# Kernel tuning notes

Measured on AMD Instinct MI355X. Metric: run time of the kernel, lower is better.

The kernel has to match this reference:

```python
import jax, jax.numpy as jnp
import numpy as np

EPS_LN = 1e-5
EPS_NORM = 1e-12


def _bilinear_matrix(in_size, out_size):
    # align_corners=True bilinear interpolation as a dense (out,in) matrix
    pos = np.arange(out_size) * (in_size - 1) / (out_size - 1)
    lo = np.floor(pos).astype(np.int64)
    hi = np.minimum(lo + 1, in_size - 1)
    frac = (pos - lo).astype(np.float32)
    M = np.zeros((out_size, in_size), np.float32)
    M[np.arange(out_size), lo] += 1.0 - frac
    M[np.arange(out_size), hi] += frac
    return jnp.asarray(M)

_M20 = _bilinear_matrix(7, 20)  # [20,7]


def _upsample(x):
    # bilinear 7x7 -> 20x20, align_corners=True: separable matmuls
    return jnp.einsum('ih,jw,nchw->ncij', _M20, _M20, x)


def _conv2d(x, w, b, stride, pad):
    out = jax.lax.conv_general_dilated(
        x, w, window_strides=(stride, stride),
        padding=[(pad, pad), (pad, pad)],
        dimension_numbers=('NCHW', 'OIHW', 'NCHW'))
    return out + b[None, :, None, None]


def _crn(x, t, ln_w, ln_b, w_t, b_t, w_s, b_s, w_m, b_m, w_l, b_l, acc_w, acc_b):
    # LayerNorm over last two dims [7,7] with elementwise affine
    mu = x.mean(axis=(-2, -1), keepdims=True)
    var = x.var(axis=(-2, -1), keepdims=True)
    xn = (x - mu) * jax.lax.rsqrt(var + EPS_LN) * ln_w + ln_b
    up = _upsample(xn)                      # [N,512,20,20]
    xs = _conv2d(up, w_s, b_s, 3, 1)        # [N,32,7,7]
    xm = _conv2d(up, w_m, b_m, 5, 9)        # [N,32,7,7]
    xl = _conv2d(up, w_l, b_l, 2, 1)        # [N,20,7,7]
    tu = _upsample(t)
    tc = _conv2d(tu, w_t, b_t, 2, 0)        # [N,16,7,7]
    cat = jnp.concatenate([xs, xm, xl, tc], axis=1)  # [N,100,7,7]
    return _conv2d(cat, acc_w, acc_b, 1, 0)          # [N,1,7,7]


def setup_inputs() -> dict:
    key = jax.random.key(0)
    ks = jax.random.split(key, 16)
    N, C, K = 512, 512, 64
    centroids = jax.random.uniform(ks[0], (K, C), dtype=jnp.float32)
    return {
        'x': jax.random.normal(ks[1], (N, C, 7, 7), dtype=jnp.float32),
        't': jax.random.normal(ks[2], (N, C, 7, 7), dtype=jnp.float32),
        'centroids': centroids,
        'conv_w': 2.0 * 100.0 * centroids,
        'conv_b': -100.0 * jnp.linalg.norm(centroids, axis=1),
        'ln_w': jnp.ones((7, 7), jnp.float32),
        'ln_b': jnp.zeros((7, 7), jnp.float32),
        'w_t': jax.random.normal(ks[3], (16, 512, 8, 8), jnp.float32) * 0.02,
        'b_t': jax.random.normal(ks[4], (16,), jnp.float32) * 0.02,
        'w_s': jax.random.normal(ks[5], (32, 512, 3, 3), jnp.float32) * 0.02,
        'b_s': jax.random.normal(ks[6], (32,), jnp.float32) * 0.02,
        'w_m': jax.random.normal(ks[7], (32, 512, 7, 7), jnp.float32) * 0.02,
        'b_m': jax.random.normal(ks[8], (32,), jnp.float32) * 0.02,
        'w_l': jax.random.normal(ks[9], (20, 512, 9, 9), jnp.float32) * 0.02,
        'b_l': jax.random.normal(ks[10], (20,), jnp.float32) * 0.02,
        'acc_w': jax.random.normal(ks[11], (1, 100, 1, 1), jnp.float32) * 0.1,
        'acc_b': jax.random.normal(ks[12], (1,), jnp.float32) * 0.1,
    }


def reference(x, t, centroids, conv_w, conv_b, ln_w, ln_b,
              w_t, b_t, w_s, b_s, w_m, b_m, w_l, b_l, acc_w, acc_b):
    N, C = x.shape[:2]
    K = centroids.shape[0]
    S = x.shape[2] * x.shape[3]  # 49

    # CRN context weights [N,1,S]
    cw = _crn(x, t, ln_w, ln_b, w_t, b_t, w_s, b_s, w_m, b_m, w_l, b_l,
              acc_w, acc_b).reshape(N, 1, S)

    # descriptor-wise L2 normalization over channel dim (F.normalize p=2 dim=1)
    nrm = jnp.sqrt(jnp.sum(x * x, axis=1, keepdims=True))
    xn = x / jnp.maximum(nrm, EPS_NORM)
    xf = xn.reshape(N, C, S)                 # [N,C,S]

    # 1x1 conv == per-pixel matmul with conv_w [K,C]
    logits = jnp.einsum('kc,ncs->nks', conv_w, xf) + conv_b[None, :, None]
    sa = jax.nn.softmax(logits, axis=1)      # softmax over clusters

    w = sa * cw                              # reweighting mask [N,K,S]
    # matmul decomposition of sum_s w*(x - c): avoids (N,K,C,S) tensor
    vlad = (jnp.einsum('nks,ncs->nkc', w, xf)
            - centroids[None] * jnp.sum(w, axis=-1)[..., None])  # [N,K,C]

    # intra-normalize over C, flatten, global L2 normalize
    vn = jnp.sqrt(jnp.sum(vlad * vlad, axis=2, keepdims=True))
    vlad = vlad / jnp.maximum(vn, EPS_NORM)
    vlad = vlad.reshape(N, K * C)
    gn = jnp.sqrt(jnp.sum(vlad * vlad, axis=1, keepdims=True))
    return vlad / jnp.maximum(gn, EPS_NORM)
```

## Files before the change

### kernel.cpp

```cpp
#include <hip/hip_runtime.h>
#include <cstdint>
#include <cstddef>


#define N_   512
#define C_   512
#define S_   49
#define CS_  25088

#define OFF_WBS   0u
#define OFF_WBM   4608u
#define OFF_WBL   29696u
#define OFF_WBT   71168u
#define OFF_BETA  103936u
#define OFF_WT    103952u
#define OFF_PLTH  136720u
#define OFF_PLTL  939536u
#define OFF_QTH   1742352u
#define OFF_QTL   2545168u
#define OFF_PWTH  3347984u
#define OFF_PWTL  3364368u
#define OFF_PB    3380752u
#define OFF_PBP   3380816u
#define OFF_MUR   3405904u
#define OFF_XS    3668048u
#define OFF_WR    3668048u
#define OFF_CWP2  16513104u
#define OFF_WSUM  19724368u
#define OFF_CENTT 19757136u

typedef __attribute__((ext_vector_type(8))) short bf16x8;
typedef __attribute__((ext_vector_type(4))) float f32x4;

__device__ __forceinline__ float wave_sum64(float v) {
  #pragma unroll
  for (int off = 32; off; off >>= 1) v += __shfl_xor(v, off, 64);
  return v;
}

__device__ __forceinline__ void bsplit(float f, short& h, short& l) {
  unsigned u = __float_as_uint(f);
  h = (short)(u >> 16);
  float hf = __uint_as_float(u & 0xffff0000u);
  l = (short)(__float_as_uint(f - hf) >> 16);
}

__device__ __forceinline__ float m20val(int r, int p) {
  float pos = (float)(r * 6) / 19.0f;
  int lo = (int)floorf(pos);
  int hi = min(lo + 1, 6);
  float fr = pos - (float)lo;
  float v = 0.f;
  if (p == lo) v += 1.f - fr;
  if (p == hi) v += fr;
  return v;
}

__global__ void k_wbar(const float* __restrict__ w_s, const float* __restrict__ w_m,
                       const float* __restrict__ w_l, const float* __restrict__ w_t,
                       const float* __restrict__ accw, const float* __restrict__ accb,
                       const float* __restrict__ b_s, const float* __restrict__ b_m,
                       const float* __restrict__ b_l, const float* __restrict__ b_t,
                       float* __restrict__ wbs, float* __restrict__ wbm,
                       float* __restrict__ wbl, float* __restrict__ wbt,
                       float* __restrict__ beta) {
  int id = blockIdx.x * 256 + threadIdx.x;
  if (id == 0) {
    float b = accb[0];
    for (int o = 0; o < 32; ++o) b = fmaf(accw[o],      b_s[o], b);
    for (int o = 0; o < 32; ++o) b = fmaf(accw[32 + o], b_m[o], b);
    for (int o = 0; o < 20; ++o) b = fmaf(accw[64 + o], b_l[o], b);
    for (int o = 0; o < 16; ++o) b = fmaf(accw[84 + o], b_t[o], b);
    beta[0] = b;
  }
  if (id < 4608) {
    int c = id / 9, uv = id % 9;
    float a = 0.f;
    for (int o = 0; o < 32; ++o) a = fmaf(accw[o], w_s[(size_t)(o * 512 + c) * 9 + uv], a);
    wbs[id] = a;
  } else if (id < 29696) {
    int i2 = id - 4608; int c = i2 / 49, uv = i2 % 49;
    float a = 0.f;
    for (int o = 0; o < 32; ++o) a = fmaf(accw[32 + o], w_m[(size_t)(o * 512 + c) * 49 + uv], a);
    wbm[i2] = a;
  } else if (id < 71168) {
    int i2 = id - 29696; int c = i2 / 81, uv = i2 % 81;
    float a = 0.f;
    for (int o = 0; o < 20; ++o) a = fmaf(accw[64 + o], w_l[(size_t)(o * 512 + c) * 81 + uv], a);
    wbl[i2] = a;
  } else {
    int i2 = id - 71168; int c = i2 / 64, uv = i2 % 64;
    float a = 0.f;
    for (int o = 0; o < 16; ++o) a = fmaf(accw[84 + o], w_t[(size_t)(o * 512 + c) * 64 + uv], a);
    wbt[i2] = a;
  }
}

__global__ void k_wt(const float* __restrict__ convw, const float* __restrict__ cent,
                     float* __restrict__ wT, float* __restrict__ centT) {
  int id = blockIdx.x * 256 + threadIdx.x;
  int id2 = id & 32767;
  int k = id2 & 63, c = id2 >> 6;
  if (id < 32768) wT[id2] = convw[(size_t)k * 512 + c];
  else            centT[id2] = cent[(size_t)k * 512 + c];
}

__global__ void k_xs(const float* __restrict__ x, float* __restrict__ xs,
                     float* __restrict__ mur) {
  int idx = blockIdx.x * 256 + threadIdx.x;
  const float* p = x + (size_t)idx * 49;
  float s1 = 0.f, s2 = 0.f;
  #pragma unroll
  for (int s = 0; s < 49; ++s) { float v = p[s]; s1 += v; s2 = fmaf(v, v, s2); }
  float m = s1 * (1.f / 49.f);
  float var = s2 * (1.f / 49.f) - m * m;
  float r = 1.f / sqrtf(var + 1e-5f);
  float* o = xs + (size_t)idx * 49;
  #pragma unroll
  for (int s = 0; s < 49; ++s) o[s] = p[s] * r;
  mur[idx] = m * r;
}

__global__ void __launch_bounds__(512) k_buildP(
    const float* __restrict__ wbs, const float* __restrict__ wbm,
    const float* __restrict__ wbl, const float* __restrict__ wbt,
    const float* __restrict__ lnw, const float* __restrict__ lnb,
    short* __restrict__ plth, short* __restrict__ pltl,
    short* __restrict__ qth,  short* __restrict__ qtl,
    short* __restrict__ pwth, short* __restrict__ pwtl,
    float* __restrict__ pbp) {
  __shared__ float M[20][7];
  __shared__ float tP[49][50];
  __shared__ float tQ[49][50];
  int c = blockIdx.x;
  int tid = threadIdx.x;
  if (tid < 140) { int r = tid / 7, p = tid % 7; M[r][p] = m20val(r, p); }
  __syncthreads();

  const float* wbsr = wbs + c * 9;
  const float* wbmr = wbm + c * 49;
  const float* wblr = wbl + c * 81;
  const float* wbtr = wbt + c * 64;

  for (int e = tid; e < 2401; e += 512) {
    int s = e / 49, q = e % 49;
    int i = q / 7, j = q % 7, pp = s / 7, qq = s % 7;

    float sumP = 0.f;
    {
      float rv[3];
      #pragma unroll
      for (int v = 0; v < 3; ++v) { int col = j * 3 - 1 + v; rv[v] = ((unsigned)col < 20u) ? M[col][qq] : 0.f; }
      #pragma unroll
      for (int u = 0; u < 3; ++u) {
        int row = i * 3 - 1 + u; float ru = ((unsigned)row < 20u) ? M[row][pp] : 0.f;
        float a = wbsr[u * 3 + 0] * rv[0];
        a = fmaf(wbsr[u * 3 + 1], rv[1], a);
        a = fmaf(wbsr[u * 3 + 2], rv[2], a);
        sumP = fmaf(ru, a, sumP);
      }
    }
    {
      float rv[7];
      #pragma unroll
      for (int v = 0; v < 7; ++v) { int col = j * 5 - 9 + v; rv[v] = ((unsigned)col < 20u) ? M[col][qq] : 0.f; }
      #pragma unroll
      for (int u = 0; u < 7; ++u) {
        int row = i * 5 - 9 + u; float ru = ((unsigned)row < 20u) ? M[row][pp] : 0.f;
        float a = 0.f;
        #pragma unroll
        for (int v = 0; v < 7; ++v) a = fmaf(wbmr[u * 7 + v], rv[v], a);
        sumP = fmaf(ru, a, sumP);
      }
    }
    {
      float rv[9];
      #pragma unroll
      for (int v = 0; v < 9; ++v) { int col = j * 2 - 1 + v; rv[v] = ((unsigned)col < 20u) ? M[col][qq] : 0.f; }
      #pragma unroll
      for (int u = 0; u < 9; ++u) {
        int row = i * 2 - 1 + u; float ru = ((unsigned)row < 20u) ? M[row][pp] : 0.f;
        float a = 0.f;
        #pragma unroll
        for (int v = 0; v < 9; ++v) a = fmaf(wblr[u * 9 + v], rv[v], a);
        sumP = fmaf(ru, a, sumP);
      }
    }
    tP[s][q] = sumP;

    float sumQ = 0.f;
    {
      float rv[8];
      #pragma unroll
      for (int v = 0; v < 8; ++v) { int col = j * 2 + v; rv[v] = ((unsigned)col < 20u) ? M[col][qq] : 0.f; }
      #pragma unroll
      for (int u = 0; u < 8; ++u) {
        int row = i * 2 + u; float ru = ((unsigned)row < 20u) ? M[row][pp] : 0.f;
        float a = 0.f;
        #pragma unroll
        for (int v = 0; v < 8; ++v) a = fmaf(wbtr[u * 8 + v], rv[v], a);
        sumQ = fmaf(ru, a, sumQ);
      }
    }
    tQ[s][q] = sumQ;
  }
  __syncthreads();

  for (int e = tid; e < 2401; e += 512) {
    int q = e / 49, s = e % 49;
    float pv = tP[s][q];
    float qv = tQ[s][q];
    int k = c * 49 + s;
    int slab = k >> 8;
    int kc = (k & 255) >> 5;
    int kg = (k >> 3) & 3;
    int off = k & 7;
    int nf = q >> 4, l15 = q & 15;
    size_t oidx = (size_t)slab * 16384 + kc * 2048 + nf * 512
                + (size_t)(kg * 16 + l15) * 8 + off;
    short h, l;
    bsplit(lnw[s] * pv, h, l); plth[oidx] = h; pltl[oidx] = l;
    bsplit(qv, h, l);          qth[oidx]  = h; qtl[oidx]  = l;
  }

  if (tid < 49) {
    int q = tid;
    float pw = 0.f, pb = 0.f;
    #pragma unroll 7
    for (int s = 0; s < 49; ++s) {
      float p = tP[s][q];
      pw = fmaf(lnw[s], p, pw);
      pb = fmaf(lnb[s], p, pb);
    }
    short h, l; bsplit(-pw, h, l);
    pwth[q * 512 + c] = h;
    pwtl[q * 512 + c] = l;
    pbp[q * 512 + c] = pb;
  }
}

__global__ void k_pb(const float* __restrict__ pbp, float* __restrict__ PB) {
  int q = blockIdx.x, lane = threadIdx.x;
  float a = 0.f;
  for (int c = lane; c < 512; c += 64) a += pbp[q * 512 + c];
  a = wave_sum64(a);
  if (lane == 0) PB[q] = a;
}

template <int SA, int SB>
__device__ __forceinline__ void mf_chunk1(const float* __restrict__ A,
                                          const short* __restrict__ Bh,
                                          const short* __restrict__ Bl,
                                          int k, int mbase, int l15, int kg,
                                          f32x4 (&acc)[4]) {
  bf16x8 ah, al;
  {
    const float* ap = A + (size_t)(mbase + l15) * SA + k + kg * 8;
    float4 v0 = *reinterpret_cast<const float4*>(ap);
    float4 v1 = *reinterpret_cast<const float4*>(ap + 4);
    float f[8] = {v0.x, v0.y, v0.z, v0.w, v1.x, v1.y, v1.z, v1.w};
    #pragma unroll
    for (int jj = 0; jj < 8; ++jj) { short hh, ll; bsplit(f[jj], hh, ll); ah[jj] = hh; al[jj] = ll; }
  }
  #pragma unroll
  for (int nf = 0; nf < 4; ++nf) {
    size_t bo = (size_t)(nf * 16 + l15) * SB + k + kg * 8;
    bf16x8 bh = *reinterpret_cast<const bf16x8*>(Bh + bo);
    bf16x8 bl = *reinterpret_cast<const bf16x8*>(Bl + bo);
    acc[nf] = __builtin_amdgcn_mfma_f32_16x16x32_bf16(ah, bh, acc[nf], 0, 0, 0);
    acc[nf] = __builtin_amdgcn_mfma_f32_16x16x32_bf16(ah, bl, acc[nf], 0, 0, 0);
    acc[nf] = __builtin_amdgcn_mfma_f32_16x16x32_bf16(al, bh, acc[nf], 0, 0, 0);
  }
}

__global__ void __launch_bounds__(64) k_cwg(
    const float* __restrict__ xs, const float* __restrict__ tin,
    const float* __restrict__ mur,
    const short* __restrict__ plth, const short* __restrict__ pltl,
    const short* __restrict__ qth,  const short* __restrict__ qtl,
    const short* __restrict__ pwth, const short* __restrict__ pwtl,
    float* __restrict__ cwp2) {
  __shared__ float at[16 * 272];
  int wgid = (blockIdx.x & 7) * 392 + (blockIdx.x >> 3);
  int slab = wgid >> 5, mt = wgid & 31;
  int lane = threadIdx.x;
  int l15 = lane & 15, kg = lane >> 4;
  int mbase = mt * 16;
  int k0 = slab * 256;

  f32x4 acc[4];
  #pragma unroll
  for (int nf = 0; nf < 4; ++nf) acc[nf] = (f32x4){0.f, 0.f, 0.f, 0.f};

  #pragma unroll 1
  for (int ph = 0; ph < 2; ++ph) {
    const float* A  = ph ? tin : xs;
    const short* Bh = ph ? qth : plth;
    const short* Bl = ph ? qtl : pltl;
    const short* bhb = Bh + (size_t)slab * 16384 + lane * 8;
    const short* blb = Bl + (size_t)slab * 16384 + lane * 8;

    bf16x8 pbh[2][4], pbl[2][4];
    #pragma unroll
    for (int nf = 0; nf < 4; ++nf) {
      pbh[0][nf] = *reinterpret_cast<const bf16x8*>(bhb + nf * 512);
      pbl[0][nf] = *reinterpret_cast<const bf16x8*>(blb + nf * 512);
    }

    __syncthreads();
    #pragma unroll
    for (int i = 0; i < 16; ++i) {
      int idx4 = i * 64 + lane;
      int row = idx4 >> 6, col4 = idx4 & 63;
      float4 v = *reinterpret_cast<const float4*>(
          &A[(size_t)(mbase + row) * CS_ + k0 + col4 * 4]);
      *reinterpret_cast<float4*>(&at[row * 272 + col4 * 4]) = v;
    }
    __syncthreads();

    #pragma unroll
    for (int kc = 0; kc < 8; ++kc) {
      int cur = kc & 1, nxt = cur ^ 1;
      if (kc < 7) {
        #pragma unroll
        for (int nf = 0; nf < 4; ++nf) {
          pbh[nxt][nf] = *reinterpret_cast<const bf16x8*>(bhb + (kc + 1) * 2048 + nf * 512);
          pbl[nxt][nf] = *reinterpret_cast<const bf16x8*>(blb + (kc + 1) * 2048 + nf * 512);
        }
      }
      bf16x8 ah, al;
      {
        const float* ap = &at[l15 * 272 + kc * 32 + kg * 8];
        float4 v0 = *reinterpret_cast<const float4*>(ap);
        float4 v1 = *reinterpret_cast<const float4*>(ap + 4);
        float f[8] = {v0.x, v0.y, v0.z, v0.w, v1.x, v1.y, v1.z, v1.w};
        #pragma unroll
        for (int jj = 0; jj < 8; ++jj) { short hh, ll; bsplit(f[jj], hh, ll); ah[jj] = hh; al[jj] = ll; }
      }
      #pragma unroll
      for (int nf = 0; nf < 4; ++nf) {
        acc[nf] = __builtin_amdgcn_mfma_f32_16x16x32_bf16(ah, pbh[cur][nf], acc[nf], 0, 0, 0);
        acc[nf] = __builtin_amdgcn_mfma_f32_16x16x32_bf16(ah, pbl[cur][nf], acc[nf], 0, 0, 0);
        acc[nf] = __builtin_amdgcn_mfma_f32_16x16x32_bf16(al, pbh[cur][nf], acc[nf], 0, 0, 0);
      }
    }
  }
  if (slab < 16)
    mf_chunk1<512, 512>(mur, pwth, pwtl, slab * 32, mbase, l15, kg, acc);

  #pragma unroll
  for (int nf = 0; nf < 4; ++nf)
    #pragma unroll
    for (int r = 0; r < 4; ++r) {
      int row = mbase + kg * 4 + r;
      int col = nf * 16 + l15;
      cwp2[(size_t)slab * 32768 + (size_t)row * 64 + col] = acc[nf][r];
    }
}

__global__ void __launch_bounds__(256) k_logits(
    const float* __restrict__ x, const float* __restrict__ wT,
    const float* __restrict__ convb, const float* __restrict__ cwp2,
    const float* __restrict__ beta, const float* __restrict__ pb,
    float* __restrict__ wr, float* __restrict__ wsum) {
  __shared__ float part[4][64][49];
  __shared__ float sqp[4][49];
  __shared__ float cw4[4 * 49];
  __shared__ float mx4[4 * 49];
  __shared__ float sm4[4 * 49];
  int n = blockIdx.x;
  int tid = threadIdx.x;
  int wu = __builtin_amdgcn_readfirstlane((int)(threadIdx.x >> 6));
  int lane = tid & 63;
  int sl = min(lane, 48);
  float* pf = &part[0][0][0];

  for (int e = tid; e < 960; e += 256) {
    int kq = e / 15, p = e % 15;
    wr[((size_t)n * 64 + kq) * 64 + 49 + p] = 0.f;
  }

  if (tid < 196) {
    int s = tid % 49, g = tid / 49;
    int st = (g < 2) ? g * 25 : 50 + (g - 2) * 24;
    int cnt = (g < 2) ? 25 : 24;
    const float* cp = cwp2 + (size_t)st * 32768 + (size_t)n * 64 + s;
    float a = 0.f;
    for (int i = 0; i < cnt; ++i) a += cp[(size_t)i * 32768];
    cw4[g * 49 + s] = a;
  }

  float acc[64];
  #pragma unroll
  for (int k = 0; k < 64; ++k) acc[k] = 0.f;
  float ssq = 0.f;
  const float* xb = x + (size_t)n * CS_ + (size_t)wu * (128 * 49);
  const float* wb = wT + wu * (128 * 64);
  #pragma unroll 1
  for (int c = 0; c < 128; ++c) {
    float xv = xb[c * 49 + sl];
    ssq = fmaf(xv, xv, ssq);
    const float* wrow = wb + c * 64;
    #pragma unroll
    for (int k = 0; k < 64; ++k) acc[k] = fmaf(wrow[k], xv, acc[k]);
  }
  if (lane < 49) {
    sqp[wu][lane] = ssq;
    #pragma unroll
    for (int k = 0; k < 64; ++k) part[wu][k][lane] = acc[k];
  }
  __syncthreads();

  float lg[16];
  int sg = tid / 49, s_ = tid % 49;
  float rnv = 0.f;
  if (tid < 196) {
    float sumsq = sqp[0][s_] + sqp[1][s_] + sqp[2][s_] + sqp[3][s_];
    rnv = 1.f / fmaxf(sqrtf(sumsq), 1e-12f);
    float mloc = -1e30f;
    #pragma unroll
    for (int kk = 0; kk < 16; ++kk) {
      int kq = sg * 16 + kk;
      float a = part[0][kq][s_] + part[1][kq][s_] + part[2][kq][s_] + part[3][kq][s_];
      lg[kk] = fmaf(a, rnv, convb[kq]);
      mloc = fmaxf(mloc, lg[kk]);
    }
    mx4[sg * 49 + s_] = mloc;
  }
  __syncthreads();
  if (tid < 196) {
    float m0 = fmaxf(fmaxf(mx4[s_], mx4[49 + s_]), fmaxf(mx4[98 + s_], mx4[147 + s_]));
    float sloc = 0.f;
    #pragma unroll
    for (int kk = 0; kk < 16; ++kk) { lg[kk] = expf(lg[kk] - m0); sloc += lg[kk]; }
    sm4[sg * 49 + s_] = sloc;
  }
  __syncthreads();
  if (tid < 196) {
    float ssum = sm4[s_] + sm4[49 + s_] + sm4[98 + s_] + sm4[147 + s_];
    float cwv = cw4[s_] + cw4[49 + s_] + cw4[98 + s_] + cw4[147 + s_] + beta[0] + pb[s_];
    float inv = cwv / ssum;
    float wrs = inv * rnv;
    #pragma unroll
    for (int kk = 0; kk < 16; ++kk) {
      int kq = sg * 16 + kk;
      wr[((size_t)n * 64 + kq) * 64 + s_] = lg[kk] * wrs;
      pf[kq * 49 + s_] = lg[kk] * inv;
    }
  }
  __syncthreads();
  if (tid < 64) {
    float a = 0.f;
    #pragma unroll 7
    for (int s = 0; s < 49; ++s) a += pf[tid * 49 + s];
    wsum[n * 64 + tid] = a;
  }
}

__global__ void __launch_bounds__(256) k_vlad(
    const float* __restrict__ x, const float* __restrict__ wr,
    const float* __restrict__ wsum, const float* __restrict__ centT,
    float* __restrict__ out) {
  __shared__ float xt[128 * 68];
  __shared__ float vl[64 * 129];
  __shared__ float sp[16][64];
  __shared__ float scal[64];
  int n = blockIdx.x;
  int tid = threadIdx.x;
  int w = tid >> 6, lane = tid & 63;
  int l15 = lane & 15, kg = lane >> 4;
  const float* xb = x + (size_t)n * CS_;
  const float* wrb = wr + (size_t)n * 4096;
  const float* wsb = wsum + n * 64;
  float* ob = out + (size_t)n * 32768;

  for (int e = tid; e < 1920; e += 256) {
    int row = e / 15, col = 49 + e % 15;
    xt[row * 68 + col] = 0.f;
  }

  float wsk[4];
  #pragma unroll
  for (int nf = 0; nf < 4; ++nf) wsk[nf] = wsb[nf * 16 + l15];
  float ssqa[4] = {0.f, 0.f, 0.f, 0.f};

  #pragma unroll 1
  for (int h = 0; h < 4; ++h) {
    int c0 = h * 128;
    __syncthreads();
    for (int e = tid; e < 6272; e += 256) {
      int row = e / 49, col = e % 49;
      xt[row * 68 + col] = xb[(size_t)c0 * 49 + e];
    }
    __syncthreads();

    f32x4 acc[2][4];
    #pragma unroll
    for (int mf = 0; mf < 2; ++mf)
      #pragma unroll
      for (int nf = 0; nf < 4; ++nf)
        acc[mf][nf] = (f32x4){0.f, 0.f, 0.f, 0.f};

    #pragma unroll
    for (int kc = 0; kc < 2; ++kc) {
      bf16x8 bh[4], bl[4];
      #pragma unroll
      for (int nf = 0; nf < 4; ++nf) {
        const float* bp = wrb + (nf * 16 + l15) * 64 + kc * 32 + kg * 8;
        float4 v0 = *reinterpret_cast<const float4*>(bp);
        float4 v1 = *reinterpret_cast<const float4*>(bp + 4);
        float f[8] = {v0.x, v0.y, v0.z, v0.w, v1.x, v1.y, v1.z, v1.w};
        #pragma unroll
        for (int jj = 0; jj < 8; ++jj) { short hh, ll; bsplit(f[jj], hh, ll); bh[nf][jj] = hh; bl[nf][jj] = ll; }
      }
      #pragma unroll
      for (int mf = 0; mf < 2; ++mf) {
        bf16x8 ah, al;
        {
          const float* ap = &xt[(w * 32 + mf * 16 + l15) * 68 + kc * 32 + kg * 8];
          float4 v0 = *reinterpret_cast<const float4*>(ap);
          float4 v1 = *reinterpret_cast<const float4*>(ap + 4);
          float f[8] = {v0.x, v0.y, v0.z, v0.w, v1.x, v1.y, v1.z, v1.w};
          #pragma unroll
          for (int jj = 0; jj < 8; ++jj) { short hh, ll; bsplit(f[jj], hh, ll); ah[jj] = hh; al[jj] = ll; }
        }
        #pragma unroll
        for (int nf = 0; nf < 4; ++nf) {
          acc[mf][nf] = __builtin_amdgcn_mfma_f32_16x16x32_bf16(ah, bh[nf], acc[mf][nf], 0, 0, 0);
          acc[mf][nf] = __builtin_amdgcn_mfma_f32_16x16x32_bf16(ah, bl[nf], acc[mf][nf], 0, 0, 0);
          acc[mf][nf] = __builtin_amdgcn_mfma_f32_16x16x32_bf16(al, bh[nf], acc[mf][nf], 0, 0, 0);
        }
      }
    }

    #pragma unroll
    for (int mf = 0; mf < 2; ++mf)
      #pragma unroll
      for (int nf = 0; nf < 4; ++nf)
        #pragma unroll
        for (int r = 0; r < 4; ++r) {
          int cc = w * 32 + mf * 16 + kg * 4 + r;
          int c = c0 + cc;
          int k = nf * 16 + l15;
          float v = fmaf(-centT[c * 64 + k], wsk[nf], acc[mf][nf][r]);
          vl[k * 129 + cc] = v;
          ssqa[nf] = fmaf(v, v, ssqa[nf]);
        }
    __syncthreads();
    #pragma unroll 4
    for (int e = tid; e < 8192; e += 256) {
      int k = e >> 7, cc = e & 127;
      ob[(size_t)k * 512 + c0 + cc] = vl[k * 129 + cc];
    }
  }

  #pragma unroll
  for (int nf = 0; nf < 4; ++nf) sp[w * 4 + kg][nf * 16 + l15] = ssqa[nf];
  __syncthreads();
  if (tid < 64) {
    float v2 = 0.f;
    #pragma unroll
    for (int j = 0; j < 16; ++j) v2 += sp[j][tid];
    float vn = sqrtf(v2);
    float den = fmaxf(vn, 1e-12f);
    float cr = vn / den; cr *= cr;
    float g = wave_sum64(cr);
    scal[tid] = 1.f / (den * fmaxf(sqrtf(g), 1e-12f));
  }
  __syncthreads();
  #pragma unroll 8
  for (int idx = tid; idx < 32768; idx += 256)
    ob[idx] *= scal[idx >> 9];
}

extern "C" void kernel_launch(void* const* d_in, const int* in_sizes, int n_in,
                              void* d_out, int out_size, void* d_ws, size_t ws_size,
                              hipStream_t stream) {
  const float* x     = (const float*)d_in[0];
  const float* t     = (const float*)d_in[1];
  const float* cent  = (const float*)d_in[2];
  const float* convw = (const float*)d_in[3];
  const float* convb = (const float*)d_in[4];
  const float* lnw   = (const float*)d_in[5];
  const float* lnb   = (const float*)d_in[6];
  const float* w_t   = (const float*)d_in[7];
  const float* b_t   = (const float*)d_in[8];
  const float* w_s   = (const float*)d_in[9];
  const float* b_s   = (const float*)d_in[10];
  const float* w_m   = (const float*)d_in[11];
  const float* b_m   = (const float*)d_in[12];
  const float* w_l   = (const float*)d_in[13];
  const float* b_l   = (const float*)d_in[14];
  const float* accw  = (const float*)d_in[15];
  const float* accb  = (const float*)d_in[16];
  float* ws  = (float*)d_ws;
  float* out = (float*)d_out;

  float* wbs  = ws + OFF_WBS;
  float* wbm  = ws + OFF_WBM;
  float* wbl  = ws + OFF_WBL;
  float* wbt  = ws + OFF_WBT;
  float* beta = ws + OFF_BETA;
  float* wT   = ws + OFF_WT;
  short* plth = (short*)(ws + OFF_PLTH);
  short* pltl = (short*)(ws + OFF_PLTL);
  short* qth  = (short*)(ws + OFF_QTH);
  short* qtl  = (short*)(ws + OFF_QTL);
  short* pwth = (short*)(ws + OFF_PWTH);
  short* pwtl = (short*)(ws + OFF_PWTL);
  float* PB   = ws + OFF_PB;
  float* pbp  = ws + OFF_PBP;
  float* mur  = ws + OFF_MUR;
  float* xs   = ws + OFF_XS;
  float* cwp2 = ws + OFF_CWP2;
  float* wr   = ws + OFF_WR;
  float* wsumb = ws + OFF_WSUM;
  float* centT = ws + OFF_CENTT;

  k_wbar<<<dim3(406), dim3(256), 0, stream>>>(w_s, w_m, w_l, w_t, accw, accb,
                                              b_s, b_m, b_l, b_t,
                                              wbs, wbm, wbl, wbt, beta);
  k_wt<<<dim3(256), dim3(256), 0, stream>>>(convw, cent, wT, centT);
  k_xs<<<dim3(1024), dim3(256), 0, stream>>>(x, xs, mur);
  hipMemsetAsync(ws + OFF_PLTH, 0, (size_t)3244032 * 4, stream);
  k_buildP<<<dim3(512), dim3(512), 0, stream>>>(wbs, wbm, wbl, wbt, lnw, lnb,
                                                plth, pltl, qth, qtl,
                                                pwth, pwtl, pbp);
  k_pb<<<dim3(49), dim3(64), 0, stream>>>(pbp, PB);
  k_cwg<<<dim3(3136), dim3(64), 0, stream>>>(xs, t, mur, plth, pltl, qth, qtl,
                                             pwth, pwtl, cwp2);
  k_logits<<<dim3(512), dim3(256), 0, stream>>>(x, wT, convb, cwp2, beta, PB, wr, wsumb);
  k_vlad<<<dim3(512), dim3(256), 0, stream>>>(x, wr, wsumb, centT, out);
}
```

Baseline: 232.4 us.

## Compute logits GEMM with 3-way split bf16 MFMA instead of scalar FMA

The logits kernel's per-pixel 512x64 projection moves from a scalar FP32 FMA loop to MFMA 16x16x32 bf16 instructions. The conv weights are pre-split into high/mid/low bf16 parts and laid out in fragment order. x is staged transposed in shared memory and split into three parts on the fly, with six cross products kept to retain near-FP32 accuracy. This removes the 64-wide register accumulator and the cross-wave reduction, at the cost of on-the-fly splitting ALU work and extra LDS staging and syncs.

```diff
diff --git a/kernel.cpp b/kernel.cpp
--- a/kernel.cpp
+++ b/kernel.cpp
@@ -13,7 +13,6 @@
 #define OFF_WBL   29696u
 #define OFF_WBT   71168u
 #define OFF_BETA  103936u
-#define OFF_WT    103952u
 #define OFF_PLTH  136720u
 #define OFF_PLTL  939536u
 #define OFF_QTH   1742352u
@@ -28,6 +27,7 @@
 #define OFF_CWP2  16513104u
 #define OFF_WSUM  19724368u
 #define OFF_CENTT 19757136u
+#define OFF_CWF   19789904u
 
 typedef __attribute__((ext_vector_type(8))) short bf16x8;
 typedef __attribute__((ext_vector_type(4))) float f32x4;
@@ -43,6 +43,18 @@
   h = (short)(u >> 16);
   float hf = __uint_as_float(u & 0xffff0000u);
   l = (short)(__float_as_uint(f - hf) >> 16);
+}
+
+__device__ __forceinline__ void bsplit3(float f, short& h, short& m, short& l) {
+  unsigned u = __float_as_uint(f);
+  h = (short)(u >> 16);
+  float hf = __uint_as_float(u & 0xffff0000u);
+  float r1 = f - hf;
+  unsigned u1 = __float_as_uint(r1);
+  m = (short)(u1 >> 16);
+  float mf = __uint_as_float(u1 & 0xffff0000u);
+  float r2 = r1 - mf;
+  l = (short)(__float_as_uint(r2) >> 16);
 }
 
 __device__ __forceinline__ float m20val(int r, int p) {
@@ -97,12 +109,21 @@
 }
 
 __global__ void k_wt(const float* __restrict__ convw, const float* __restrict__ cent,
-                     float* __restrict__ wT, float* __restrict__ centT) {
+                     short* __restrict__ cwfh, short* __restrict__ cwfm,
+                     short* __restrict__ cwfl, float* __restrict__ centT) {
   int id = blockIdx.x * 256 + threadIdx.x;
-  int id2 = id & 32767;
-  int k = id2 & 63, c = id2 >> 6;
-  if (id < 32768) wT[id2] = convw[(size_t)k * 512 + c];
-  else            centT[id2] = cent[(size_t)k * 512 + c];
+  if (id < 32768) {
+    int k = id >> 9, c = id & 511;
+    short h, m, l; bsplit3(convw[(size_t)k * 512 + c], h, m, l);
+    int kc = c >> 5, kg = (c >> 3) & 3, off = c & 7;
+    int w = k >> 4, l15 = k & 15;
+    int idx = ((kc * 4 + w) * 64 + kg * 16 + l15) * 8 + off;
+    cwfh[idx] = h; cwfm[idx] = m; cwfl[idx] = l;
+  } else {
+    int id2 = id - 32768;
+    int k = id2 & 63, c = id2 >> 6;
+    centT[id2] = cent[(size_t)k * 512 + c];
+  }
 }
 
 __global__ void k_xs(const float* __restrict__ x, float* __restrict__ xs,
@@ -359,25 +380,32 @@
 }
 
 __global__ void __launch_bounds__(256) k_logits(
-    const float* __restrict__ x, const float* __restrict__ wT,
+    const float* __restrict__ x,
+    const short* __restrict__ cwfh, const short* __restrict__ cwfm,
+    const short* __restrict__ cwfl,
     const float* __restrict__ convb, const float* __restrict__ cwp2,
     const float* __restrict__ beta, const float* __restrict__ pb,
     float* __restrict__ wr, float* __restrict__ wsum) {
-  __shared__ float part[4][64][49];
+  __shared__ float xt[64 * 140];
+  __shared__ float part2[64 * 52];
   __shared__ float sqp[4][49];
   __shared__ float cw4[4 * 49];
   __shared__ float mx4[4 * 49];
   __shared__ float sm4[4 * 49];
   int n = blockIdx.x;
   int tid = threadIdx.x;
-  int wu = __builtin_amdgcn_readfirstlane((int)(threadIdx.x >> 6));
-  int lane = tid & 63;
-  int sl = min(lane, 48);
-  float* pf = &part[0][0][0];
+  int w = tid >> 6, lane = tid & 63;
+  int l15 = lane & 15, kg = lane >> 4;
+  float* pf = part2;
+  const float* xb = x + (size_t)n * CS_;
 
   for (int e = tid; e < 960; e += 256) {
     int kq = e / 15, p = e % 15;
     wr[((size_t)n * 64 + kq) * 64 + 49 + p] = 0.f;
+  }
+  for (int e = tid; e < 1920; e += 256) {
+    int row = 49 + e / 128, col = e % 128;
+    xt[row * 140 + col] = 0.f;
   }
 
   if (tid < 196) {
@@ -390,25 +418,67 @@
     cw4[g * 49 + s] = a;
   }
 
-  float acc[64];
-  #pragma unroll
-  for (int k = 0; k < 64; ++k) acc[k] = 0.f;
-  float ssq = 0.f;
-  const float* xb = x + (size_t)n * CS_ + (size_t)wu * (128 * 49);
-  const float* wb = wT + wu * (128 * 64);
+  int scol = tid % 49, sgrp = tid / 49;
+  float ssql = 0.f;
+  f32x4 acc[4];
+  #pragma unroll
+  for (int nf = 0; nf < 4; ++nf) acc[nf] = (f32x4){0.f, 0.f, 0.f, 0.f};
+
   #pragma unroll 1
-  for (int c = 0; c < 128; ++c) {
-    float xv = xb[c * 49 + sl];
-    ssq = fmaf(xv, xv, ssq);
-    const float* wrow = wb + c * 64;
-    #pragma unroll
-    for (int k = 0; k < 64; ++k) acc[k] = fmaf(wrow[k], xv, acc[k]);
-  }
-  if (lane < 49) {
-    sqp[wu][lane] = ssq;
-    #pragma unroll
-    for (int k = 0; k < 64; ++k) part[wu][k][lane] = acc[k];
-  }
+  for (int h = 0; h < 4; ++h) {
+    int c0 = h * 128;
+    __syncthreads();
+    for (int e = tid; e < 6272; e += 256) {
+      int c_row = e / 49, col = e % 49;
+      xt[col * 140 + c_row] = xb[(size_t)c0 * 49 + e];
+    }
+    __syncthreads();
+
+    if (tid < 196) {
+      #pragma unroll 8
+      for (int j = 0; j < 32; ++j) {
+        float v = xt[scol * 140 + sgrp * 32 + j];
+        ssql = fmaf(v, v, ssql);
+      }
+    }
+
+    #pragma unroll
+    for (int kcl = 0; kcl < 4; ++kcl) {
+      int kc = h * 4 + kcl;
+      bf16x8 ah = *reinterpret_cast<const bf16x8*>(cwfh + ((kc * 4 + w) * 64 + lane) * 8);
+      bf16x8 am = *reinterpret_cast<const bf16x8*>(cwfm + ((kc * 4 + w) * 64 + lane) * 8);
+      bf16x8 al = *reinterpret_cast<const bf16x8*>(cwfl + ((kc * 4 + w) * 64 + lane) * 8);
+      #pragma unroll
+      for (int nf = 0; nf < 4; ++nf) {
+        const float* bp = &xt[(nf * 16 + l15) * 140 + kcl * 32 + kg * 8];
+        float4 v0 = *reinterpret_cast<const float4*>(bp);
+        float4 v1 = *reinterpret_cast<const float4*>(bp + 4);
+        float f[8] = {v0.x, v0.y, v0.z, v0.w, v1.x, v1.y, v1.z, v1.w};
+        bf16x8 bh, bm, bl;
+        #pragma unroll
+        for (int jj = 0; jj < 8; ++jj) {
+          short hh, mm, ll; bsplit3(f[jj], hh, mm, ll);
+          bh[jj] = hh; bm[jj] = mm; bl[jj] = ll;
+        }
+        acc[nf] = __builtin_amdgcn_mfma_f32_16x16x32_bf16(ah, bh, acc[nf], 0, 0, 0);
+        acc[nf] = __builtin_amdgcn_mfma_f32_16x16x32_bf16(ah, bm, acc[nf], 0, 0, 0);
+        acc[nf] = __builtin_amdgcn_mfma_f32_16x16x32_bf16(am, bh, acc[nf], 0, 0, 0);
+        acc[nf] = __builtin_amdgcn_mfma_f32_16x16x32_bf16(ah, bl, acc[nf], 0, 0, 0);
+        acc[nf] = __builtin_amdgcn_mfma_f32_16x16x32_bf16(am, bm, acc[nf], 0, 0, 0);
+        acc[nf] = __builtin_amdgcn_mfma_f32_16x16x32_bf16(al, bh, acc[nf], 0, 0, 0);
+      }
+    }
+  }
+  __syncthreads();
+
+  #pragma unroll
+  for (int nf = 0; nf < 4; ++nf)
+    #pragma unroll
+    for (int r = 0; r < 4; ++r) {
+      int s = nf * 16 + l15;
+      if (s < 49) part2[(w * 16 + kg * 4 + r) * 52 + s] = acc[nf][r];
+    }
+  if (tid < 196) sqp[sgrp][scol] = ssql;
   __syncthreads();
 
   float lg[16];
@@ -421,8 +491,7 @@
     #pragma unroll
     for (int kk = 0; kk < 16; ++kk) {
       int kq = sg * 16 + kk;
-      float a = part[0][kq][s_] + part[1][kq][s_] + part[2][kq][s_] + part[3][kq][s_];
-      lg[kk] = fmaf(a, rnv, convb[kq]);
+      lg[kk] = fmaf(part2[kq * 52 + s_], rnv, convb[kq]);
       mloc = fmaxf(mloc, lg[kk]);
     }
     mx4[sg * 49 + s_] = mloc;
@@ -601,7 +670,9 @@
   float* wbl  = ws + OFF_WBL;
   float* wbt  = ws + OFF_WBT;
   float* beta = ws + OFF_BETA;
-  float* wT   = ws + OFF_WT;
+  short* cwfh = (short*)(ws + OFF_CWF);
+  short* cwfm = (short*)(ws + OFF_CWF + 16384);
+  short* cwfl = (short*)(ws + OFF_CWF + 32768);
   short* plth = (short*)(ws + OFF_PLTH);
   short* pltl = (short*)(ws + OFF_PLTL);
   short* qth  = (short*)(ws + OFF_QTH);
@@ -620,7 +691,7 @@
   k_wbar<<<dim3(406), dim3(256), 0, stream>>>(w_s, w_m, w_l, w_t, accw, accb,
                                               b_s, b_m, b_l, b_t,
                                               wbs, wbm, wbl, wbt, beta);
-  k_wt<<<dim3(256), dim3(256), 0, stream>>>(convw, cent, wT, centT);
+  k_wt<<<dim3(256), dim3(256), 0, stream>>>(convw, cent, cwfh, cwfm, cwfl, centT);
   k_xs<<<dim3(1024), dim3(256), 0, stream>>>(x, xs, mur);
   hipMemsetAsync(ws + OFF_PLTH, 0, (size_t)3244032 * 4, stream);
   k_buildP<<<dim3(512), dim3(512), 0, stream>>>(wbs, wbm, wbl, wbt, lnw, lnb,
@@ -629,6 +700,7 @@
   k_pb<<<dim3(49), dim3(64), 0, stream>>>(pbp, PB);
   k_cwg<<<dim3(3136), dim3(64), 0, stream>>>(xs, t, mur, plth, pltl, qth, qtl,
                                              pwth, pwtl, cwp2);
-  k_logits<<<dim3(512), dim3(256), 0, stream>>>(x, wT, convb, cwp2, beta, PB, wr, wsumb);
+  k_logits<<<dim3(512), dim3(256), 0, stream>>>(x, cwfh, cwfm, cwfl, convb, cwp2,
+                                                beta, PB, wr, wsumb);
   k_vlad<<<dim3(512), dim3(256), 0, stream>>>(x, wr, wsumb, centT, out);
 }
```

Result: faster. 209.6 us (median of 2 runs) (-9.8%).
